# Optimization experiments

Measured on AMD Instinct MI355X. Metric: run time of the kernel, lower is better.

The kernel has to match this reference:

```python
import jax, jax.numpy as jnp
import numpy as np

N_NODES, T, C_IN, B = 207, 12, 4, 4
NT = N_NODES * T
D, H = 96, 4
HD = D // H
FF = 4 * D
ENC_L, DEC_L = 4, 1
N_MASK = int(NT * 0.75)
N_UNMASK = NT - N_MASK
MAX_NEIGH = 40
ATTN_SCALE = 1.0 / float(np.sqrt(HD))
SQRT_D = float(np.sqrt(D))


def _ln(x, g, b, eps=1e-5):
    m = jnp.mean(x, -1, keepdims=True)
    v = jnp.mean((x - m) ** 2, -1, keepdims=True)
    return (x - m) * jax.lax.rsqrt(v + eps) * g + b


def _transformer(x, attn_mask, layers):
    # x: [B, S, D]; attn_mask: [S, S] bool (True = disallowed) or None.
    x = x * SQRT_D  # nn.Transformer-style input scaling
    def step(h, p):
        aw, ab, W1, B1, W2, B2, LN = p
        Bq, S, _ = h.shape
        q = (h @ aw[0] + ab[0]).reshape(Bq, S, H, HD)
        k = (h @ aw[1] + ab[1]).reshape(Bq, S, H, HD)
        v = (h @ aw[2] + ab[2]).reshape(Bq, S, H, HD)
        scores = jnp.einsum('bqhd,bkhd->bhqk', q, k) * ATTN_SCALE
        if attn_mask is not None:
            scores = jnp.where(attn_mask, jnp.float32(-1e30), scores)
        probs = jax.nn.softmax(scores, axis=-1)
        o = jnp.einsum('bhqk,bkhd->bqhd', probs, v).reshape(Bq, S, D)
        h = _ln(h + o @ aw[3] + ab[3], LN[0, 0], LN[0, 1])  # post-norm (torch default)
        f = jax.nn.relu(h @ W1 + B1) @ W2 + B2
        h = _ln(h + f, LN[1, 0], LN[1, 1])
        return h, None
    x, _ = jax.lax.scan(step, x, layers)
    return x


def _layer_params(key, nlayers):
    ks = jax.random.split(key, 3)
    attn_w = jax.random.normal(ks[0], (nlayers, 4, D, D), jnp.float32) / float(np.sqrt(D))
    w1 = jax.random.normal(ks[1], (nlayers, D, FF), jnp.float32) / float(np.sqrt(D))
    w2 = jax.random.normal(ks[2], (nlayers, FF, D), jnp.float32) / float(np.sqrt(FF))
    ln = jnp.broadcast_to(jnp.stack([jnp.ones(D), jnp.zeros(D)]), (nlayers, 2, 2, D)).astype(jnp.float32)
    return (attn_w, jnp.zeros((nlayers, 4, D), jnp.float32), w1,
            jnp.zeros((nlayers, FF), jnp.float32), w2, jnp.zeros((nlayers, D), jnp.float32), ln)


def setup_inputs() -> dict:
    key = jax.random.key(0)
    ks = jax.random.split(key, 12)
    rng = np.random.default_rng(42)
    perm = rng.permutation(NT)
    masked_idx = jnp.asarray(np.sort(perm[:N_MASK]), jnp.int32)
    unmasked_idx = jnp.asarray(np.sort(perm[N_MASK:]), jnp.int32)
    ea = _layer_params(ks[3], ENC_L)
    da = _layer_params(ks[4], DEC_L)
    return dict(
        history_data=jax.random.uniform(ks[0], (B, T, N_NODES, C_IN), jnp.float32),
        unmasked_idx=unmasked_idx, masked_idx=masked_idx,
        nodevec1=jax.random.normal(ks[1], (N_NODES, 10), jnp.float32),
        nodevec2=jax.random.normal(ks[2], (10, N_NODES), jnp.float32),
        dim_w=jax.random.normal(ks[5], (1, D), jnp.float32),
        dim_b=jnp.zeros((D,), jnp.float32),
        pos_emb=jax.random.uniform(ks[6], (NT, D), jnp.float32, -0.02, 0.02),
        tod_w=jax.random.normal(ks[7], (1, D), jnp.float32) * 0.02,
        tod_b=jnp.zeros((D,), jnp.float32),
        dow_w=jax.random.normal(ks[8], (1, D), jnp.float32) * 0.02,
        dow_b=jnp.zeros((D,), jnp.float32),
        mask_token=jax.random.normal(ks[9], (D,), jnp.float32) * 0.02,
        enc_attn_w=ea[0], enc_attn_b=ea[1], enc_ffn_w1=ea[2], enc_ffn_b1=ea[3],
        enc_ffn_w2=ea[4], enc_ffn_b2=ea[5], enc_ln=ea[6],
        enc_norm_g=jnp.ones((D,), jnp.float32), enc_norm_b=jnp.zeros((D,), jnp.float32),
        e2d_w=jax.random.normal(ks[10], (D, D), jnp.float32) / float(np.sqrt(D)),
        e2d_b=jnp.zeros((D,), jnp.float32),
        dec_attn_w=da[0], dec_attn_b=da[1], dec_ffn_w1=da[2], dec_ffn_b1=da[3],
        dec_ffn_w2=da[4], dec_ffn_b2=da[5], dec_ln=da[6],
        dec_norm_g=jnp.ones((D,), jnp.float32), dec_norm_b=jnp.zeros((D,), jnp.float32),
        out_w=jax.random.normal(ks[11], (D, 1), jnp.float32) / float(np.sqrt(D)),
        out_b=jnp.zeros((1,), jnp.float32),
    )


def reference(history_data, unmasked_idx, masked_idx, nodevec1, nodevec2,
              dim_w, dim_b, pos_emb, tod_w, tod_b, dow_w, dow_b, mask_token,
              enc_attn_w, enc_attn_b, enc_ffn_w1, enc_ffn_b1, enc_ffn_w2, enc_ffn_b2, enc_ln,
              enc_norm_g, enc_norm_b, e2d_w, e2d_b,
              dec_attn_w, dec_attn_b, dec_ffn_w1, dec_ffn_b1, dec_ffn_w2, dec_ffn_b2, dec_ln,
              dec_norm_g, dec_norm_b, out_w, out_b):
    hist = jnp.transpose(history_data, (0, 2, 3, 1))  # [B, N, C, T]
    tod = hist[:, :, 3:4, :].reshape(B, NT, 1)
    dow = hist[:, :, 2:3, :].reshape(B, NT, 1)
    # --- adaptive graph: softmax(relu(v1 v2)), threshold + top-40, straight-through ---
    A = jax.nn.softmax(jax.nn.relu(nodevec1 @ nodevec2), axis=1)
    kth = -jnp.sort(-A, axis=1)[:, MAX_NEIGH:MAX_NEIGH + 1]  # (MAX_NEIGH+1)-th largest per row
    keep = jnp.logical_and(A > 1.0 / N_NODES, A > kth).astype(A.dtype)
    bin_mask = jax.lax.stop_gradient(keep - A) + A
    adpA = A * bin_mask
    adpA_full = jnp.repeat(jnp.repeat(adpA, T, axis=0), T, axis=1)  # [NT, NT] block structure
    # --- embed + positional/temporal encoding ---
    x = jnp.transpose(hist[:, :, 0:1, :], (0, 1, 3, 2)) @ dim_w + dim_b  # [B, N, T, D]
    token = x.reshape(B, NT, D) + pos_emb + (tod @ tod_w + tod_b) + (dow @ dow_w + dow_b)
    # --- encoder over unmasked tokens with graph-derived attention mask ---
    enc_in = token[:, unmasked_idx, :]
    A_sub = adpA_full[unmasked_idx][:, unmasked_idx]
    attn_mask = A_sub == 0  # ~A.bool(): True = disallowed
    h = _transformer(enc_in, attn_mask,
                     (enc_attn_w, enc_attn_b, enc_ffn_w1, enc_ffn_b1, enc_ffn_w2, enc_ffn_b2, enc_ln))
    h = _ln(h, enc_norm_g, enc_norm_b)
    # --- decoder ---
    h = h @ e2d_w + e2d_b
    h_masked = (mask_token[None, None, :] + pos_emb[masked_idx]
                + (tod[:, masked_idx] @ tod_w + tod_b)
                + (dow[:, masked_idx] @ dow_w + dow_b))  # [B, N_MASK, D]
    full = jnp.concatenate([h, h_masked], axis=1)  # [B, NT, D]
    full = _transformer(full, None,
                        (dec_attn_w, dec_attn_b, dec_ffn_w1, dec_ffn_b1, dec_ffn_w2, dec_ffn_b2, dec_ln))
    full = _ln(full, dec_norm_g, dec_norm_b)
    recon = full @ out_w + out_b  # [B, NT, 1]
    recon_masked = recon[:, N_UNMASK:, :]
    label = jnp.transpose(hist, (0, 1, 3, 2))[:, :, :, 0].reshape(B, NT, 1)
    label_masked = label[:, masked_idx, :]
    return recon_masked, label_masked
```

## Files before the change

kernel.cpp:

```cpp
#include <hip/hip_runtime.h>
#include <math.h>

#define N_NODES 207
#define T_STEPS 12
#define NT 2484
#define BQ 4
#define DIM 96
#define NH 4
#define HD 24
#define FFD 384
#define N_MASK 1863
#define N_UNMASK 621
#define MAX_NEIGH 40
#define ATTN_SCALE 0.20412414523193154f
#define SQRT_DF 9.797958971132712f
#define KT 256
#define NMW 20
#define NBH 16

static inline int cdiv(int a, int b) { return (a + b - 1) / b; }

__global__ __launch_bounds__(256) void adj_kernel(const float* __restrict__ nv1,
                                                  const float* __restrict__ nv2,
                                                  float* __restrict__ keep) {
    int r = blockIdx.x, t = threadIdx.x;
    __shared__ float a[N_NODES];
    __shared__ float red[256];
    __shared__ int   redi[256];
    __shared__ int   taken[N_NODES];
    __shared__ float v1[10];
    __shared__ float kth;
    if (t < 10) v1[t] = nv1[r * 10 + t];
    __syncthreads();
    if (t < N_NODES) {
        float s = 0.f;
#pragma unroll
        for (int c = 0; c < 10; ++c) s += v1[c] * nv2[c * N_NODES + t];
        a[t] = fmaxf(s, 0.f);
        taken[t] = 0;
    }
    __syncthreads();
    red[t] = (t < N_NODES) ? a[t] : -3e38f;
    __syncthreads();
    for (int s = 128; s > 0; s >>= 1) {
        if (t < s) red[t] = fmaxf(red[t], red[t + s]);
        __syncthreads();
    }
    float mx = red[0];
    __syncthreads();
    float e = 0.f;
    if (t < N_NODES) e = __expf(a[t] - mx);
    red[t] = e;
    __syncthreads();
    for (int s = 128; s > 0; s >>= 1) {
        if (t < s) red[t] += red[t + s];
        __syncthreads();
    }
    float inv = 1.f / red[0];
    __syncthreads();
    if (t < N_NODES) a[t] = e * inv;
    __syncthreads();
    for (int round = 0; round <= MAX_NEIGH; ++round) {
        red[t]  = (t < N_NODES && !taken[t]) ? a[t] : -1.f;
        redi[t] = t;
        __syncthreads();
        for (int s = 128; s > 0; s >>= 1) {
            if (t < s && red[t + s] > red[t]) { red[t] = red[t + s]; redi[t] = redi[t + s]; }
            __syncthreads();
        }
        if (t == 0) {
            taken[redi[0]] = 1;
            if (round == MAX_NEIGH) kth = red[0];
        }
        __syncthreads();
    }
    if (t < N_NODES) {
        float av = a[t];
        keep[r * N_NODES + t] = (av > (1.f / 207.f) && av > kth) ? 1.f : 0.f;
    }
}

__global__ void maskbits_kernel(const float* __restrict__ keep, const int* __restrict__ uidx,
                                unsigned int* __restrict__ mw) {
    int q = blockIdx.x;
    int w = threadIdx.x;
    if (w >= NMW) return;
    const float* krow = keep + (uidx[q] / T_STEPS) * N_NODES;
    unsigned int word = 0;
    for (int j = 0; j < 32; ++j) {
        int k = w * 32 + j;
        if (k < N_UNMASK && krow[uidx[k] / T_STEPS] != 0.f) word |= (1u << j);
    }
    mw[q * NMW + w] = word;
}

__global__ void encin_kernel(const float* __restrict__ hist, const int* __restrict__ uidx,
                             const float* __restrict__ dim_w, const float* __restrict__ dim_b,
                             const float* __restrict__ pos,
                             const float* __restrict__ tod_w, const float* __restrict__ tod_b,
                             const float* __restrict__ dow_w, const float* __restrict__ dow_b,
                             float* __restrict__ h) {
    int idx = blockIdx.x * blockDim.x + threadIdx.x;
    if (idx >= BQ * N_UNMASK * DIM) return;
    int d = idx % DIM;
    int q = (idx / DIM) % N_UNMASK;
    int b = idx / (DIM * N_UNMASK);
    int u = uidx[q];
    int n = u / T_STEPS, t = u % T_STEPS;
    const float* hp = hist + ((size_t)(b * T_STEPS + t) * N_NODES + n) * 4;
    float h0 = hp[0], dw = hp[2], td = hp[3];
    float val = h0 * dim_w[d] + dim_b[d] + pos[u * DIM + d]
              + td * tod_w[d] + tod_b[d] + dw * dow_w[d] + dow_b[d];
    h[idx] = val * SQRT_DF;
}

__global__ void hmasked_kernel(const float* __restrict__ hist, const int* __restrict__ midx,
                               const float* __restrict__ mask_token, const float* __restrict__ pos,
                               const float* __restrict__ tod_w, const float* __restrict__ tod_b,
                               const float* __restrict__ dow_w, const float* __restrict__ dow_b,
                               float* __restrict__ full) {
    int idx = blockIdx.x * blockDim.x + threadIdx.x;
    if (idx >= BQ * N_MASK * DIM) return;
    int d = idx % DIM;
    int j = (idx / DIM) % N_MASK;
    int b = idx / (DIM * N_MASK);
    int m = midx[j];
    int n = m / T_STEPS, t = m % T_STEPS;
    const float* hp = hist + ((size_t)(b * T_STEPS + t) * N_NODES + n) * 4;
    float dw = hp[2], td = hp[3];
    float val = mask_token[d] + pos[m * DIM + d]
              + td * tod_w[d] + tod_b[d] + dw * dow_w[d] + dow_b[d];
    full[((size_t)(b * NT) + N_UNMASK + j) * DIM + d] = val * SQRT_DF;
}

__global__ void label_kernel(const float* __restrict__ hist, const int* __restrict__ midx,
                             float* __restrict__ out) {
    int idx = blockIdx.x * blockDim.x + threadIdx.x;
    if (idx >= BQ * N_MASK) return;
    int j = idx % N_MASK;
    int b = idx / N_MASK;
    int m = midx[j];
    int n = m / T_STEPS, t = m % T_STEPS;
    out[BQ * N_MASK + idx] = hist[((size_t)(b * T_STEPS + t) * N_NODES + n) * 4 + 0];
}

#define ACCROW(accv, av)                                          \
    accv.x += av.x*w0.x + av.y*w1.x + av.z*w2.x + av.w*w3.x;      \
    accv.y += av.x*w0.y + av.y*w1.y + av.z*w2.y + av.w*w3.y;      \
    accv.z += av.x*w0.z + av.y*w1.z + av.z*w2.z + av.w*w3.z;      \
    accv.w += av.x*w0.w + av.y*w1.w + av.z*w2.w + av.w*w3.w;

template<int WMODE, int LNA>
__global__ __launch_bounds__(256) void tgemm_kernel(const float* __restrict__ A,
                                                    const float* __restrict__ W,
                                                    const float* __restrict__ bias,
                                                    const float* __restrict__ res,
                                                    float* __restrict__ C,
                                                    int M, int N, int K, int gm,
                                                    int relu, float scale, int rmode,
                                                    int omode,
                                                    const float* __restrict__ g1,
                                                    const float* __restrict__ b1,
                                                    const float* __restrict__ g2,
                                                    const float* __restrict__ b2,
                                                    float* __restrict__ wb) {
    __shared__ float As[64][100];
    __shared__ float Ws[96][64];
    __shared__ float lred[64][4];
    __shared__ float lmv[64][2];
    int tid = threadIdx.x;
    int bm = blockIdx.x % gm;
    int bn = blockIdx.x / gm;
    int m0 = bm * 64, n0 = bn * 64;
    int tn4 = (tid & 15) * 4;
    int tm4 = (tid >> 4) * 4;
    float4 acc0 = {0,0,0,0}, acc1 = {0,0,0,0}, acc2 = {0,0,0,0}, acc3 = {0,0,0,0};

    for (int kc = 0; kc < K; kc += 96) {
        if (kc) __syncthreads();
#pragma unroll
        for (int i = 0; i < 6; ++i) {
            int f = i * 256 + tid;
            int r = f / 24, c4 = (f % 24) * 4;
            float4 v = {0,0,0,0};
            if (m0 + r < M) v = *(const float4*)(A + (size_t)(m0 + r) * K + kc + c4);
            *(float4*)&As[r][c4] = v;
        }
#pragma unroll
        for (int i = 0; i < 6; ++i) {
            int f = i * 256 + tid;
            int kr = f >> 4, n4 = (f & 15) * 4;
            int gn = n0 + n4;
            float4 v = {0,0,0,0};
            if (gn < N) {
                if (WMODE == 0) {
                    v = *(const float4*)(W + (size_t)(kc + kr) * N + gn);
                } else {
                    int gg = gn / 96, nc = gn - gg * 96;
                    v = *(const float4*)(W + (size_t)gg * 9216 + (kc + kr) * 96 + nc);
                }
            }
            *(float4*)&Ws[kr][n4] = v;
        }
        __syncthreads();

        if (LNA > 0 && kc == 0) {
#pragma unroll
            for (int pass = 0; pass < LNA; ++pass) {
                const float* lg = pass ? g2 : g1;
                const float* lb = pass ? b2 : b1;
                int row = tid >> 2, part = tid & 3;
                float s = 0.f;
                for (int c = part * 24; c < part * 24 + 24; ++c) s += As[row][c];
                lred[row][part] = s;
                __syncthreads();
                float mean = (lred[row][0] + lred[row][1] + lred[row][2] + lred[row][3]) * (1.f / 96.f);
                float s2 = 0.f;
                for (int c = part * 24; c < part * 24 + 24; ++c) {
                    float d = As[row][c] - mean; s2 += d * d;
                }
                __syncthreads();
                lred[row][part] = s2;
                __syncthreads();
                if (part == 0) {
                    float var = (lred[row][0] + lred[row][1] + lred[row][2] + lred[row][3]) * (1.f / 96.f);
                    lmv[row][0] = mean;
                    lmv[row][1] = rsqrtf(var + 1e-5f);
                }
                __syncthreads();
#pragma unroll
                for (int i = 0; i < 6; ++i) {
                    int f = i * 256 + tid;
                    int r = f / 24, c4 = (f % 24) * 4;
                    float mn = lmv[r][0], rsd = lmv[r][1];
                    float4 v = *(float4*)&As[r][c4];
                    v.x = (v.x - mn) * rsd * lg[c4 + 0] + lb[c4 + 0];
                    v.y = (v.y - mn) * rsd * lg[c4 + 1] + lb[c4 + 1];
                    v.z = (v.z - mn) * rsd * lg[c4 + 2] + lb[c4 + 2];
                    v.w = (v.w - mn) * rsd * lg[c4 + 3] + lb[c4 + 3];
                    *(float4*)&As[r][c4] = v;
                }
                __syncthreads();
            }
            if (wb && bn == 0) {
#pragma unroll
                for (int i = 0; i < 6; ++i) {
                    int f = i * 256 + tid;
                    int r = f / 24, c4 = (f % 24) * 4;
                    if (m0 + r < M)
                        *(float4*)(wb + (size_t)(m0 + r) * 96 + c4) = *(const float4*)&As[r][c4];
                }
            }
        }

#pragma unroll 4
        for (int k = 0; k < 96; k += 4) {
            float4 a0 = *(const float4*)&As[tm4 + 0][k];
            float4 a1 = *(const float4*)&As[tm4 + 1][k];
            float4 a2 = *(const float4*)&As[tm4 + 2][k];
            float4 a3 = *(const float4*)&As[tm4 + 3][k];
            float4 w0 = *(const float4*)&Ws[k + 0][tn4];
            float4 w1 = *(const float4*)&Ws[k + 1][tn4];
            float4 w2 = *(const float4*)&Ws[k + 2][tn4];
            float4 w3 = *(const float4*)&Ws[k + 3][tn4];
            ACCROW(acc0, a0)
            ACCROW(acc1, a1)
            ACCROW(acc2, a2)
            ACCROW(acc3, a3)
        }
    }

    int gn = n0 + tn4;
    if (gn >= N) return;
    float4 bv = *(const float4*)(bias + gn);
    float4 av[4] = {acc0, acc1, acc2, acc3};
#pragma unroll
    for (int i = 0; i < 4; ++i) {
        int grow = m0 + tm4 + i;
        if (grow >= M) break;
        float4 acc = av[i];
        acc.x += bv.x; acc.y += bv.y; acc.z += bv.z; acc.w += bv.w;
        if (res) {
            int rr = grow;
            if (rmode) { int bb = grow / N_MASK; rr = bb * NT + N_UNMASK + (grow - bb * N_MASK); }
            float4 rv = *(const float4*)(res + (size_t)rr * N + gn);
            acc.x += rv.x; acc.y += rv.y; acc.z += rv.z; acc.w += rv.w;
        }
        if (relu) {
            acc.x = fmaxf(acc.x, 0.f); acc.y = fmaxf(acc.y, 0.f);
            acc.z = fmaxf(acc.z, 0.f); acc.w = fmaxf(acc.w, 0.f);
        }
        acc.x *= scale; acc.y *= scale; acc.z *= scale; acc.w *= scale;
        int orow = grow;
        if (omode) { int bb = grow / N_UNMASK; orow = bb * NT + (grow - bb * N_UNMASK); }
        *(float4*)(C + (size_t)orow * N + gn) = acc;
    }
}

template<int QPL>
__global__ __launch_bounds__(256) void fattn_kernel(const float* __restrict__ Qp,
                                                    const float* __restrict__ Kp,
                                                    const float* __restrict__ Vp,
                                                    float* __restrict__ Pm,
                                                    float* __restrict__ Pl,
                                                    float* __restrict__ Pacc,
                                                    const unsigned int* __restrict__ maskw,
                                                    int swz,
                                                    int S, int Sq, int qoff,
                                                    int nqt, int NS, int rs) {
    __shared__ float smem[12288];
    float* Ks = smem;
    float* Vs = smem + 6144;

    int t = threadIdx.x;
    int w = t >> 6, lane = t & 63;
    int bid = blockIdx.x;
    int ns, qt, hh, b;
    if (swz) {
        int xcd = bid & 7, slot = bid >> 3;
        int spb = nqt * NS;
        int bh = xcd + 8 * (slot / spb);
        int r = slot % spb;
        qt = r / NS; ns = r % NS;
        b = bh >> 2; hh = bh & 3;
    } else {
        ns = bid % NS; int r1 = bid / NS;
        qt = r1 % nqt; r1 /= nqt;
        hh = r1 % NH; b = r1 / NH;
    }

    float qr[QPL][HD];
    bool qvalid[QPL];
#pragma unroll
    for (int h = 0; h < QPL; ++h) {
        int qidx = qt * (64 * QPL) + h * 64 + lane;
        qvalid[h] = qidx < Sq;
        if (qvalid[h]) {
            const float* qp = Qp + ((size_t)(b * S + qoff + qidx)) * rs + hh * HD;
#pragma unroll
            for (int i = 0; i < 6; ++i) {
                float4 v = *(const float4*)(qp + i * 4);
                qr[h][i*4+0] = v.x; qr[h][i*4+1] = v.y;
                qr[h][i*4+2] = v.z; qr[h][i*4+3] = v.w;
            }
        } else {
#pragma unroll
            for (int d = 0; d < HD; ++d) qr[h][d] = 0.f;
        }
    }

    float m[QPL], l[QPL];
    float acc[QPL][HD];
#pragma unroll
    for (int h = 0; h < QPL; ++h) {
        m[h] = -1e30f; l[h] = 0.f;
#pragma unroll
        for (int d = 0; d < HD; ++d) acc[h][d] = 0.f;
    }

    int ntile = (S + KT - 1) / KT;
    for (int c = ns; c < ntile; c += NS) {
        __syncthreads();
        int base_k = c * KT;
#pragma unroll
        for (int i = 0; i < 6; ++i) {
            int fi = i * 256 + t;
            int row = fi / 6, cc = fi - row * 6;
            int gk = base_k + row;
            float4 kv = {0,0,0,0};
            float4 vv = {0,0,0,0};
            if (gk < S) {
                size_t roff = ((size_t)(b * S + gk)) * rs + hh * HD + cc * 4;
                kv = *(const float4*)(Kp + roff);
                vv = *(const float4*)(Vp + roff);
            }
            *(float4*)(Ks + row * HD + cc * 4) = kv;
            *(float4*)(Vs + row * HD + cc * 4) = vv;
        }
        __syncthreads();

        unsigned int mw0 = ~0u, mw1 = ~0u;
        if (QPL == 1 && maskw) {
            int qidx = qt * 64 + lane;
            if (qidx < Sq) {
                int wi = c * 8 + w * 2;
                mw0 = (wi     < NMW) ? maskw[qidx * NMW + wi]     : 0u;
                mw1 = (wi + 1 < NMW) ? maskw[qidx * NMW + wi + 1] : 0u;
            }
        }

        for (int g = 0; g < 16; ++g) {
            float sgrp[QPL][4];
            float pv[QPL][4];
#pragma unroll
            for (int j = 0; j < 4; ++j) {
                int j2 = g * 4 + j;
                int kk = (w << 6) + j2;
                int gk = base_k + kk;
                const float4* kr = (const float4*)(Ks + kk * HD);
                float d0[QPL];
#pragma unroll
                for (int h = 0; h < QPL; ++h) d0[h] = 0.f;
#pragma unroll
                for (int i = 0; i < 6; ++i) {
                    float4 kv = kr[i];
#pragma unroll
                    for (int h = 0; h < QPL; ++h) {
                        d0[h] += qr[h][i*4+0]*kv.x + qr[h][i*4+1]*kv.y
                               + qr[h][i*4+2]*kv.z + qr[h][i*4+3]*kv.w;
                    }
                }
#pragma unroll
                for (int h = 0; h < QPL; ++h) {
                    float s = d0[h] * ATTN_SCALE;
                    if (QPL == 1 && maskw) {
                        unsigned int wsel = (j2 & 32) ? mw1 : mw0;
                        if (!((wsel >> (j2 & 31)) & 1u)) s = -1e30f;
                    }
                    if (gk >= S) s = -INFINITY;
                    sgrp[h][j] = s;
                }
            }
#pragma unroll
            for (int h = 0; h < QPL; ++h) {
                float gmx = fmaxf(fmaxf(sgrp[h][0], sgrp[h][1]),
                                  fmaxf(sgrp[h][2], sgrp[h][3]));
                if (gmx > m[h]) {
                    float f = __expf(m[h] - gmx);
                    l[h] *= f;
#pragma unroll
                    for (int d = 0; d < HD; ++d) acc[h][d] *= f;
                    m[h] = gmx;
                }
#pragma unroll
                for (int j = 0; j < 4; ++j) {
                    float p = __expf(sgrp[h][j] - m[h]);
                    pv[h][j] = p;
                    l[h] += p;
                }
            }
#pragma unroll
            for (int j = 0; j < 4; ++j) {
                int kk = (w << 6) + g * 4 + j;
                const float4* vr = (const float4*)(Vs + kk * HD);
#pragma unroll
                for (int i = 0; i < 6; ++i) {
                    float4 vv = vr[i];
#pragma unroll
                    for (int h = 0; h < QPL; ++h) {
                        acc[h][i*4+0] += pv[h][j]*vv.x;
                        acc[h][i*4+1] += pv[h][j]*vv.y;
                        acc[h][i*4+2] += pv[h][j]*vv.z;
                        acc[h][i*4+3] += pv[h][j]*vv.w;
                    }
                }
            }
        }
    }

#pragma unroll
    for (int h = 0; h < QPL; ++h) {
        __syncthreads();
        float* my = smem + (size_t)(w * 64 + lane) * 27;
        my[0] = m[h]; my[1] = l[h];
#pragma unroll
        for (int d = 0; d < HD; ++d) my[2 + d] = acc[h][d];
        __syncthreads();
        if (t < 64) {
            int qidx = qt * (64 * QPL) + h * 64 + t;
            if (qidx < Sq) {
                float M2 = -INFINITY;
#pragma unroll
                for (int w2 = 0; w2 < 4; ++w2)
                    M2 = fmaxf(M2, smem[(size_t)(w2 * 64 + t) * 27]);
                float L = 0.f;
                float o[HD];
#pragma unroll
                for (int d = 0; d < HD; ++d) o[d] = 0.f;
#pragma unroll
                for (int w2 = 0; w2 < 4; ++w2) {
                    const float* pp = smem + (size_t)(w2 * 64 + t) * 27;
                    float f = __expf(pp[0] - M2);
                    L += pp[1] * f;
#pragma unroll
                    for (int d = 0; d < HD; ++d) o[d] += pp[2 + d] * f;
                }
                int bh = b * NH + hh;
                size_t pq = ((size_t)(ns * NBH + bh)) * Sq + qidx;
                Pm[pq] = M2;
                Pl[pq] = L;
                float* pa = Pacc + pq * 24;
#pragma unroll
                for (int i = 0; i < 6; ++i)
                    *(float4*)(pa + i * 4) = make_float4(o[i*4+0], o[i*4+1],
                                                         o[i*4+2], o[i*4+3]);
            }
        }
    }
}

__global__ __launch_bounds__(256) void attn_combine_kernel(const float* __restrict__ Pm,
                                                           const float* __restrict__ Pl,
                                                           const float* __restrict__ Pacc,
                                                           float* __restrict__ O,
                                                           int Sq, int NS) {
    int tid = blockIdx.x * 256 + threadIdx.x;
    if (tid >= NBH * Sq * 6) return;
    int d4 = tid % 6;
    int q  = (tid / 6) % Sq;
    int bh = tid / (6 * Sq);
    float M = -1e30f;
    for (int ns = 0; ns < NS; ++ns)
        M = fmaxf(M, Pm[((size_t)(ns * NBH + bh)) * Sq + q]);
    float L = 0.f;
    float ax = 0.f, ay = 0.f, az = 0.f, aw = 0.f;
    for (int ns = 0; ns < NS; ++ns) {
        size_t pq = ((size_t)(ns * NBH + bh)) * Sq + q;
        float wgt = __expf(Pm[pq] - M);
        L += wgt * Pl[pq];
        float4 f0 = *(const float4*)(Pacc + pq * 24 + d4 * 4);
        ax += wgt * f0.x; ay += wgt * f0.y;
        az += wgt * f0.z; aw += wgt * f0.w;
    }
    float inv = 1.f / L;
    int b = bh >> 2, hh = bh & 3;
    float* op = O + ((size_t)(b * Sq + q)) * DIM + hh * HD + d4 * 4;
    *(float4*)op = make_float4(ax * inv, ay * inv, az * inv, aw * inv);
}

__global__ __launch_bounds__(256) void tail_kernel(const float* __restrict__ X,
                                                   const float* __restrict__ g1,
                                                   const float* __restrict__ b1,
                                                   const float* __restrict__ g2,
                                                   const float* __restrict__ b2,
                                                   const float* __restrict__ ow,
                                                   const float* __restrict__ ob,
                                                   float* __restrict__ out, int Mtail) {
    int row = blockIdx.x * 4 + (threadIdx.x >> 6);
    if (row >= Mtail) return;
    int lane = threadIdx.x & 63;
    bool lo = lane < 32;
    const float* x = X + (size_t)row * DIM;
    float x0 = x[lane];
    float x1 = lo ? x[64 + lane] : 0.f;
    float s = x0 + x1;
#pragma unroll
    for (int o = 32; o; o >>= 1) s += __shfl_xor(s, o);
    float mean = s * (1.f / DIM);
    float d0 = x0 - mean;
    float d1 = lo ? (x1 - mean) : 0.f;
    float v = d0 * d0 + d1 * d1;
#pragma unroll
    for (int o = 32; o; o >>= 1) v += __shfl_xor(v, o);
    float rs = rsqrtf(v * (1.f / DIM) + 1e-5f);
    float y0 = d0 * rs * g1[lane] + b1[lane];
    float y1 = lo ? (d1 * rs * g1[64 + lane] + b1[64 + lane]) : 0.f;
    s = y0 + y1;
#pragma unroll
    for (int o = 32; o; o >>= 1) s += __shfl_xor(s, o);
    mean = s * (1.f / DIM);
    d0 = y0 - mean;
    d1 = lo ? (y1 - mean) : 0.f;
    v = d0 * d0 + d1 * d1;
#pragma unroll
    for (int o = 32; o; o >>= 1) v += __shfl_xor(v, o);
    rs = rsqrtf(v * (1.f / DIM) + 1e-5f);
    float z0 = d0 * rs * g2[lane] + b2[lane];
    float z1 = lo ? (d1 * rs * g2[64 + lane] + b2[64 + lane]) : 0.f;
    float a = z0 * ow[lane] + (lo ? z1 * ow[64 + lane] : 0.f);
#pragma unroll
    for (int o = 32; o; o >>= 1) a += __shfl_xor(a, o);
    if (lane == 0) out[row] = a + ob[0];
}

extern "C" void kernel_launch(void* const* d_in, const int* in_sizes, int n_in,
                              void* d_out, int out_size, void* d_ws, size_t ws_size,
                              hipStream_t stream) {
    const float* hist   = (const float*)d_in[0];
    const int*   uidx   = (const int*)d_in[1];
    const int*   midx   = (const int*)d_in[2];
    const float* nv1    = (const float*)d_in[3];
    const float* nv2    = (const float*)d_in[4];
    const float* dim_w  = (const float*)d_in[5];
    const float* dim_b  = (const float*)d_in[6];
    const float* pos    = (const float*)d_in[7];
    const float* tod_w  = (const float*)d_in[8];
    const float* tod_b  = (const float*)d_in[9];
    const float* dow_w  = (const float*)d_in[10];
    const float* dow_b  = (const float*)d_in[11];
    const float* mtok   = (const float*)d_in[12];
    const float* eaw    = (const float*)d_in[13];
    const float* eab    = (const float*)d_in[14];
    const float* ew1    = (const float*)d_in[15];
    const float* eb1    = (const float*)d_in[16];
    const float* ew2    = (const float*)d_in[17];
    const float* eb2    = (const float*)d_in[18];
    const float* eln    = (const float*)d_in[19];
    const float* eng    = (const float*)d_in[20];
    const float* enb    = (const float*)d_in[21];
    const float* e2dw   = (const float*)d_in[22];
    const float* e2db   = (const float*)d_in[23];
    const float* daw    = (const float*)d_in[24];
    const float* dab    = (const float*)d_in[25];
    const float* dw1    = (const float*)d_in[26];
    const float* db1    = (const float*)d_in[27];
    const float* dw2    = (const float*)d_in[28];
    const float* db2    = (const float*)d_in[29];
    const float* dln    = (const float*)d_in[30];
    const float* dng    = (const float*)d_in[31];
    const float* dnb    = (const float*)d_in[32];
    const float* ow     = (const float*)d_in[33];
    const float* ob     = (const float*)d_in[34];

    float* ws = (float*)d_ws;
    float*        keep  = ws;
    unsigned int* maskw = (unsigned int*)(ws + 44032);
    float* eh = ws + 56576;
    float* e1 = ws + 295040;
    float* e2 = ws + 1248896;
    float* et = ws + 1487360;
    float* fh = ws + 1725824;
    float* qf = ws + 2679680;
    float* dh = ws + 5541248;
    float* dt = ws + 6256640;
    float* PaccE = ws + 5541248;
    float* PmE   = ws + 6256640;
    float* PlE   = ws + 6286448;
    float* PaccD = ws + 56576;
    float* PmD   = ws + 1487360;
    float* PlD   = ws + 1546976;
    float* dY = ws + 56576;
    float* dZ = ws + 771968;

    float* outp = (float*)d_out;
    const int ME = BQ * N_UNMASK;
    const int MD = BQ * NT;
    const int MT = BQ * N_MASK;
    const int gmE = cdiv(ME, 64);
    const int gmD = cdiv(MD, 64);
    const int gmT = cdiv(MT, 64);
    const int NSE = 3, NSD = 2;
    const int nqtE = 10;
    const int nqtD = 15;

    adj_kernel<<<N_NODES, 256, 0, stream>>>(nv1, nv2, keep);
    maskbits_kernel<<<N_UNMASK, 32, 0, stream>>>(keep, uidx, maskw);
    encin_kernel<<<cdiv(ME * DIM, 256), 256, 0, stream>>>(
        hist, uidx, dim_w, dim_b, pos, tod_w, tod_b, dow_w, dow_b, eh);
    label_kernel<<<cdiv(MT, 256), 256, 0, stream>>>(hist, midx, outp);

    for (int l = 0; l < 4; ++l) {
        const float* aw = eaw + (size_t)l * 4 * DIM * DIM;
        const float* ab = eab + (size_t)l * 4 * DIM;
        if (l == 0) {
            tgemm_kernel<1,0><<<gmE * 5, 256, 0, stream>>>(
                eh, aw, ab, nullptr, e1, ME, 288, 96, gmE, 0, 1.f, 0, 0,
                nullptr, nullptr, nullptr, nullptr, nullptr);
        } else {
            tgemm_kernel<1,1><<<gmE * 5, 256, 0, stream>>>(
                et, aw, ab, nullptr, e1, ME, 288, 96, gmE, 0, 1.f, 0, 0,
                eln + (size_t)((l - 1) * 4 + 2) * DIM,
                eln + (size_t)((l - 1) * 4 + 3) * DIM,
                nullptr, nullptr, eh);
        }
        fattn_kernel<1><<<NBH * nqtE * NSE, 256, 0, stream>>>(
            e1, e1 + 96, e1 + 192, PmE, PlE, PaccE, maskw, 1,
            N_UNMASK, N_UNMASK, 0, nqtE, NSE, 288);
        attn_combine_kernel<<<cdiv(NBH * N_UNMASK * 6, 256), 256, 0, stream>>>(
            PmE, PlE, PaccE, e2, N_UNMASK, NSE);
        tgemm_kernel<0,0><<<gmE * 2, 256, 0, stream>>>(
            e2, aw + 3 * DIM * DIM, ab + 3 * DIM, eh, et, ME, 96, 96, gmE, 0, 1.f, 0, 0,
            nullptr, nullptr, nullptr, nullptr, nullptr);
        tgemm_kernel<0,1><<<gmE * 6, 256, 0, stream>>>(
            et, ew1 + (size_t)l * DIM * FFD, eb1 + (size_t)l * FFD, nullptr, e1,
            ME, FFD, 96, gmE, 1, 1.f, 0, 0,
            eln + (size_t)(l * 4 + 0) * DIM, eln + (size_t)(l * 4 + 1) * DIM,
            nullptr, nullptr, eh);
        tgemm_kernel<0,0><<<gmE * 2, 256, 0, stream>>>(
            e1, ew2 + (size_t)l * FFD * DIM, eb2 + (size_t)l * DIM, eh, et,
            ME, 96, FFD, gmE, 0, 1.f, 0, 0,
            nullptr, nullptr, nullptr, nullptr, nullptr);
    }
    tgemm_kernel<0,2><<<gmE * 2, 256, 0, stream>>>(
        et, e2dw, e2db, nullptr, fh, ME, 96, 96, gmE, 0, SQRT_DF, 0, 1,
        eln + (size_t)(3 * 4 + 2) * DIM, eln + (size_t)(3 * 4 + 3) * DIM,
        eng, enb, nullptr);
    hmasked_kernel<<<cdiv(MT * DIM, 256), 256, 0, stream>>>(
        hist, midx, mtok, pos, tod_w, tod_b, dow_w, dow_b, fh);

    tgemm_kernel<1,0><<<gmD * 5, 256, 0, stream>>>(
        fh, daw, dab, nullptr, qf, MD, 288, 96, gmD, 0, 1.f, 0, 0,
        nullptr, nullptr, nullptr, nullptr, nullptr);
    fattn_kernel<2><<<NBH * nqtD * NSD, 256, 0, stream>>>(
        qf, qf + 96, qf + 192, PmD, PlD, PaccD, nullptr, 1,
        NT, N_MASK, N_UNMASK, nqtD, NSD, 288);
    attn_combine_kernel<<<cdiv(NBH * N_MASK * 6, 256), 256, 0, stream>>>(
        PmD, PlD, PaccD, dt, N_MASK, NSD);
    tgemm_kernel<0,0><<<gmT * 2, 256, 0, stream>>>(
        dt, daw + 3 * DIM * DIM, dab + 3 * DIM, fh, dY, MT, 96, 96, gmT, 0, 1.f, 1, 0,
        nullptr, nullptr, nullptr, nullptr, nullptr);
    tgemm_kernel<0,1><<<gmT * 6, 256, 0, stream>>>(
        dY, dw1, db1, nullptr, qf, MT, FFD, 96, gmT, 1, 1.f, 0, 0,
        dln + 0 * DIM, dln + 1 * DIM, nullptr, nullptr, dZ);
    tgemm_kernel<0,0><<<gmT * 2, 256, 0, stream>>>(
        qf, dw2, db2, dZ, dh, MT, 96, FFD, gmT, 0, 1.f, 0, 0,
        nullptr, nullptr, nullptr, nullptr, nullptr);
    tail_kernel<<<cdiv(MT, 4), 256, 0, stream>>>(
        dh, dln + 2 * DIM, dln + 3 * DIM, dng, dnb, ow, ob, outp, MT);
}
```

Measured before the change: 683.6 us.

## Fuse attention split-combine into output-projection GEMM A-tile load

Removes the separate attn_combine kernel and does the log-sum-exp merge of the split-key partial results inside the output-projection GEMM, while the A tile is loaded into shared memory. Each thread merges one row-head pair and writes it straight into As. This drops one launch per layer and the global write and re-read of the combined attention output. In exchange each GEMM tile recomputes the combine once per N-block (two blocks), holds a 24-float register array per thread, and loads Pacc with less coalescing.

```diff
diff --git a/kernel.cpp b/kernel.cpp
--- a/kernel.cpp
+++ b/kernel.cpp
@@ -150,7 +150,7 @@
     accv.z += av.x*w0.z + av.y*w1.z + av.z*w2.z + av.w*w3.z;      \
     accv.w += av.x*w0.w + av.y*w1.w + av.z*w2.w + av.w*w3.w;
 
-template<int WMODE, int LNA>
+template<int WMODE, int LNA, int CMB>
 __global__ __launch_bounds__(256) void tgemm_kernel(const float* __restrict__ A,
                                                     const float* __restrict__ W,
                                                     const float* __restrict__ bias,
@@ -163,7 +163,11 @@
                                                     const float* __restrict__ b1,
                                                     const float* __restrict__ g2,
                                                     const float* __restrict__ b2,
-                                                    float* __restrict__ wb) {
+                                                    float* __restrict__ wb,
+                                                    const float* __restrict__ Pm2,
+                                                    const float* __restrict__ Pl2,
+                                                    const float* __restrict__ Pacc2,
+                                                    int Sq2, int NS2) {
     __shared__ float As[64][100];
     __shared__ float Ws[96][64];
     __shared__ float lred[64][4];
@@ -178,13 +182,48 @@
 
     for (int kc = 0; kc < K; kc += 96) {
         if (kc) __syncthreads();
-#pragma unroll
-        for (int i = 0; i < 6; ++i) {
-            int f = i * 256 + tid;
-            int r = f / 24, c4 = (f % 24) * 4;
-            float4 v = {0,0,0,0};
-            if (m0 + r < M) v = *(const float4*)(A + (size_t)(m0 + r) * K + kc + c4);
-            *(float4*)&As[r][c4] = v;
+        if (CMB) {
+            int r = tid >> 2, hh2 = tid & 3;
+            int grow = m0 + r;
+            float o[24];
+#pragma unroll
+            for (int d = 0; d < 24; ++d) o[d] = 0.f;
+            float Lv = 1.f;
+            if (grow < M) {
+                int bb = grow / Sq2, q = grow - bb * Sq2;
+                int bh = bb * NH + hh2;
+                float Mx = -1e30f;
+                for (int ns = 0; ns < NS2; ++ns)
+                    Mx = fmaxf(Mx, Pm2[((size_t)(ns * NBH + bh)) * Sq2 + q]);
+                Lv = 0.f;
+                for (int ns = 0; ns < NS2; ++ns) {
+                    size_t pq = ((size_t)(ns * NBH + bh)) * Sq2 + q;
+                    float wgt = __expf(Pm2[pq] - Mx);
+                    Lv += wgt * Pl2[pq];
+                    const float* pa = Pacc2 + pq * 24;
+#pragma unroll
+                    for (int i = 0; i < 6; ++i) {
+                        float4 f = *(const float4*)(pa + i * 4);
+                        o[i*4+0] += wgt * f.x; o[i*4+1] += wgt * f.y;
+                        o[i*4+2] += wgt * f.z; o[i*4+3] += wgt * f.w;
+                    }
+                }
+            }
+            float inv = 1.f / Lv;
+#pragma unroll
+            for (int i = 0; i < 6; ++i)
+                *(float4*)&As[r][hh2 * 24 + i * 4] =
+                    make_float4(o[i*4+0] * inv, o[i*4+1] * inv,
+                                o[i*4+2] * inv, o[i*4+3] * inv);
+        } else {
+#pragma unroll
+            for (int i = 0; i < 6; ++i) {
+                int f = i * 256 + tid;
+                int r = f / 24, c4 = (f % 24) * 4;
+                float4 v = {0,0,0,0};
+                if (m0 + r < M) v = *(const float4*)(A + (size_t)(m0 + r) * K + kc + c4);
+                *(float4*)&As[r][c4] = v;
+            }
         }
 #pragma unroll
         for (int i = 0; i < 6; ++i) {
@@ -497,35 +536,6 @@
             }
         }
     }
-}
-
-__global__ __launch_bounds__(256) void attn_combine_kernel(const float* __restrict__ Pm,
-                                                           const float* __restrict__ Pl,
-                                                           const float* __restrict__ Pacc,
-                                                           float* __restrict__ O,
-                                                           int Sq, int NS) {
-    int tid = blockIdx.x * 256 + threadIdx.x;
-    if (tid >= NBH * Sq * 6) return;
-    int d4 = tid % 6;
-    int q  = (tid / 6) % Sq;
-    int bh = tid / (6 * Sq);
-    float M = -1e30f;
-    for (int ns = 0; ns < NS; ++ns)
-        M = fmaxf(M, Pm[((size_t)(ns * NBH + bh)) * Sq + q]);
-    float L = 0.f;
-    float ax = 0.f, ay = 0.f, az = 0.f, aw = 0.f;
-    for (int ns = 0; ns < NS; ++ns) {
-        size_t pq = ((size_t)(ns * NBH + bh)) * Sq + q;
-        float wgt = __expf(Pm[pq] - M);
-        L += wgt * Pl[pq];
-        float4 f0 = *(const float4*)(Pacc + pq * 24 + d4 * 4);
-        ax += wgt * f0.x; ay += wgt * f0.y;
-        az += wgt * f0.z; aw += wgt * f0.w;
-    }
-    float inv = 1.f / L;
-    int b = bh >> 2, hh = bh & 3;
-    float* op = O + ((size_t)(b * Sq + q)) * DIM + hh * HD + d4 * 4;
-    *(float4*)op = make_float4(ax * inv, ay * inv, az * inv, aw * inv);
 }
 
 __global__ __launch_bounds__(256) void tail_kernel(const float* __restrict__ X,
@@ -617,7 +627,6 @@
     unsigned int* maskw = (unsigned int*)(ws + 44032);
     float* eh = ws + 56576;
     float* e1 = ws + 295040;
-    float* e2 = ws + 1248896;
     float* et = ws + 1487360;
     float* fh = ws + 1725824;
     float* qf = ws + 2679680;
@@ -629,7 +638,6 @@
     float* PaccD = ws + 56576;
     float* PmD   = ws + 1487360;
     float* PlD   = ws + 1546976;
-    float* dY = ws + 56576;
     float* dZ = ws + 771968;
 
     float* outp = (float*)d_out;
@@ -653,58 +661,66 @@
         const float* aw = eaw + (size_t)l * 4 * DIM * DIM;
         const float* ab = eab + (size_t)l * 4 * DIM;
         if (l == 0) {
-            tgemm_kernel<1,0><<<gmE * 5, 256, 0, stream>>>(
+            tgemm_kernel<1,0,0><<<gmE * 5, 256, 0, stream>>>(
                 eh, aw, ab, nullptr, e1, ME, 288, 96, gmE, 0, 1.f, 0, 0,
-                nullptr, nullptr, nullptr, nullptr, nullptr);
+                nullptr, nullptr, nullptr, nullptr, nullptr,
+                nullptr, nullptr, nullptr, 0, 0);
         } else {
-            tgemm_kernel<1,1><<<gmE * 5, 256, 0, stream>>>(
+            tgemm_kernel<1,1,0><<<gmE * 5, 256, 0, stream>>>(
                 et, aw, ab, nullptr, e1, ME, 288, 96, gmE, 0, 1.f, 0, 0,
                 eln + (size_t)((l - 1) * 4 + 2) * DIM,
                 eln + (size_t)((l - 1) * 4 + 3) * DIM,
-                nullptr, nullptr, eh);
+                nullptr, nullptr, eh,
+                nullptr, nullptr, nullptr, 0, 0);
         }
         fattn_kernel<1><<<NBH * nqtE * NSE, 256, 0, stream>>>(
             e1, e1 + 96, e1 + 192, PmE, PlE, PaccE, maskw, 1,
             N_UNMASK, N_UNMASK, 0, nqtE, NSE, 288);
-        attn_combine_kernel<<<cdiv(NBH * N_UNMASK * 6, 256), 256, 0, stream>>>(
-            PmE, PlE, PaccE, e2, N_UNMASK, NSE);
-        tgemm_kernel<0,0><<<gmE * 2, 256, 0, stream>>>(
-            e2, aw + 3 * DIM * DIM, ab + 3 * DIM, eh, et, ME, 96, 96, gmE, 0, 1.f, 0, 0,
-            nullptr, nullptr, nullptr, nullptr, nullptr);
-        tgemm_kernel<0,1><<<gmE * 6, 256, 0, stream>>>(
+        tgemm_kernel<0,0,1><<<gmE * 2, 256, 0, stream>>>(
+            nullptr, aw + 3 * DIM * DIM, ab + 3 * DIM, eh, et, ME, 96, 96, gmE,
+            0, 1.f, 0, 0,
+            nullptr, nullptr, nullptr, nullptr, nullptr,
+            PmE, PlE, PaccE, N_UNMASK, NSE);
+        tgemm_kernel<0,1,0><<<gmE * 6, 256, 0, stream>>>(
             et, ew1 + (size_t)l * DIM * FFD, eb1 + (size_t)l * FFD, nullptr, e1,
             ME, FFD, 96, gmE, 1, 1.f, 0, 0,
             eln + (size_t)(l * 4 + 0) * DIM, eln + (size_t)(l * 4 + 1) * DIM,
-            nullptr, nullptr, eh);
-        tgemm_kernel<0,0><<<gmE * 2, 256, 0, stream>>>(
+            nullptr, nullptr, eh,
+            nullptr, nullptr, nullptr, 0, 0);
+        tgemm_kernel<0,0,0><<<gmE * 2, 256, 0, stream>>>(
             e1, ew2 + (size_t)l * FFD * DIM, eb2 + (size_t)l * DIM, eh, et,
             ME, 96, FFD, gmE, 0, 1.f, 0, 0,
-            nullptr, nullptr, nullptr, nullptr, nullptr);
-    }
-    tgemm_kernel<0,2><<<gmE * 2, 256, 0, stream>>>(
+            nullptr, nullptr, nullptr, nullptr, nullptr,
+            nullptr, nullptr, nullptr, 0, 0);
+    }
+    tgemm_kernel<0,2,0><<<gmE * 2, 256, 0, stream>>>(
         et, e2dw, e2db, nullptr, fh, ME, 96, 96, gmE, 0, SQRT_DF, 0, 1,
         eln + (size_t)(3 * 4 + 2) * DIM, eln + (size_t)(3 * 4 + 3) * DIM,
-        eng, enb, nullptr);
+        eng, enb, nullptr,
+        nullptr, nullptr, nullptr, 0, 0);
     hmasked_kernel<<<cdiv(MT * DIM, 256), 256, 0, stream>>>(
         hist, midx, mtok, pos, tod_w, tod_b, dow_w, dow_b, fh);
 
-    tgemm_kernel<1,0><<<gmD * 5, 256, 0, stream>>>(
+    tgemm_kernel<1,0,0><<<gmD * 5, 256, 0, stream>>>(
         fh, daw, dab, nullptr, qf, MD, 288, 96, gmD, 0, 1.f, 0, 0,
-        nullptr, nullptr, nullptr, nullptr, nullptr);
+        nullptr, nullptr, nullptr, nullptr, nullptr,
+        nullptr, nullptr, nullptr, 0, 0);
     fattn_kernel<2><<<NBH * nqtD * NSD, 256, 0, stream>>>(
         qf, qf + 96, qf + 192, PmD, PlD, PaccD, nullptr, 1,
         NT, N_MASK, N_UNMASK, nqtD, NSD, 288);
-    attn_combine_kernel<<<cdiv(NBH * N_MASK * 6, 256), 256, 0, stream>>>(
-        PmD, PlD, PaccD, dt, N_MASK, NSD);
-    tgemm_kernel<0,0><<<gmT * 2, 256, 0, stream>>>(
-        dt, daw + 3 * DIM * DIM, dab + 3 * DIM, fh, dY, MT, 96, 96, gmT, 0, 1.f, 1, 0,
-        nullptr, nullptr, nullptr, nullptr, nullptr);
-    tgemm_kernel<0,1><<<gmT * 6, 256, 0, stream>>>(
-        dY, dw1, db1, nullptr, qf, MT, FFD, 96, gmT, 1, 1.f, 0, 0,
-        dln + 0 * DIM, dln + 1 * DIM, nullptr, nullptr, dZ);
-    tgemm_kernel<0,0><<<gmT * 2, 256, 0, stream>>>(
+    tgemm_kernel<0,0,1><<<gmT * 2, 256, 0, stream>>>(
+        nullptr, daw + 3 * DIM * DIM, dab + 3 * DIM, fh, dt, MT, 96, 96, gmT,
+        0, 1.f, 1, 0,
+        nullptr, nullptr, nullptr, nullptr, nullptr,
+        PmD, PlD, PaccD, N_MASK, NSD);
+    tgemm_kernel<0,1,0><<<gmT * 6, 256, 0, stream>>>(
+        dt, dw1, db1, nullptr, qf, MT, FFD, 96, gmT, 1, 1.f, 0, 0,
+        dln + 0 * DIM, dln + 1 * DIM, nullptr, nullptr, dZ,
+        nullptr, nullptr, nullptr, 0, 0);
+    tgemm_kernel<0,0,0><<<gmT * 2, 256, 0, stream>>>(
         qf, dw2, db2, dZ, dh, MT, 96, FFD, gmT, 0, 1.f, 0, 0,
-        nullptr, nullptr, nullptr, nullptr, nullptr);
+        nullptr, nullptr, nullptr, nullptr, nullptr,
+        nullptr, nullptr, nullptr, 0, 0);
     tail_kernel<<<cdiv(MT, 4), 256, 0, stream>>>(
         dh, dln + 2 * DIM, dln + 3 * DIM, dng, dnb, ow, ob, outp, MT);
 }
```

Result: no change. 672.4 us, median of 2 (-1.7%).
